# Kernel tuning notes

Hardware: AMD Instinct MI355X
Metric: run time of the kernel (lower is better)

## Reference

```python
import jax, jax.numpy as jnp
import numpy as np
import math


def _conv1x1(x, w, b):
    # x: [B,C,H,W], w: [O,C], b: [O] -> [B,O,H,W]
    return jnp.einsum('oc,bchw->bohw', w, x) + b[None, :, None, None]


def _attn_branch(x, f_w, f_b, g_w, g_b, h_w, h_b, gamma):
    B, C, H, W = x.shape
    N = H * W
    k_dim = C // 8
    f = _conv1x1(x, f_w, f_b).reshape(B, k_dim, N)  # [B,k,N]
    g = _conv1x1(x, g_w, g_b).reshape(B, k_dim, N)  # [B,k,N]
    # attention[b, n, m] = sum_k f[b,k,n] * g[b,k,m] / sqrt(k_dim)
    scores = jnp.einsum('bkn,bkm->bnm', f, g) / math.sqrt(k_dim)
    attn = jax.nn.softmax(scores, axis=2)  # softmax over last dim (dim=2)
    h = _conv1x1(x, h_w, h_b).reshape(B, C, N)  # [B,C,N]
    sa_map = jnp.einsum('bcn,bnm->bcm', h, attn).reshape(B, C, H, W)
    return gamma[0] * sa_map + x


def setup_inputs() -> dict:
    key = jax.random.key(0)
    ks = jax.random.split(key, 8)
    B, C, H, W = 4, 256, 64, 64
    kd = C // 8
    scale_in = 1.0 / math.sqrt(C)
    return {
        'x1': jax.random.normal(ks[0], (B, C, H, W), jnp.float32),
        'x2': jax.random.normal(ks[1], (B, C, H, W), jnp.float32),
        'f_w': jax.random.normal(ks[2], (kd, C), jnp.float32) * scale_in,
        'f_b': jnp.zeros((kd,), jnp.float32),
        'g_w': jax.random.normal(ks[3], (kd, C), jnp.float32) * scale_in,
        'g_b': jnp.zeros((kd,), jnp.float32),
        'h1_w': jax.random.normal(ks[4], (C, C), jnp.float32) * scale_in,
        'h1_b': jnp.zeros((C,), jnp.float32),
        'h2_w': jax.random.normal(ks[5], (C, C), jnp.float32) * scale_in,
        'h2_b': jnp.zeros((C,), jnp.float32),
        'gamma1': jax.random.normal(ks[6], (1,), jnp.float32),
        'gamma2': jax.random.normal(ks[7], (1,), jnp.float32),
    }


def reference(x1, x2, f_w, f_b, g_w, g_b, h1_w, h1_b, h2_w, h2_b, gamma1, gamma2):
    y1 = _attn_branch(x1, f_w, f_b, g_w, g_b, h1_w, h1_b, gamma1)
    y2 = _attn_branch(x2, f_w, f_b, g_w, g_b, h2_w, h2_b, gamma2)
    return (y1, y2)
```

## Files before the change

kernel.cpp:

```cpp
#include <hip/hip_runtime.h>
#include <math.h>

#define NDIM 4096
#define CDIM 256
#define KD   32
#define SCALE 0.17677669529663687f
#define SHIFT 8.0f

typedef __attribute__((ext_vector_type(8))) short short8;
typedef __attribute__((ext_vector_type(4))) float f32x4;
typedef unsigned short u16;
typedef unsigned int u32;

__device__ __forceinline__ u32 f2bf(float x) {
  union { float f; u32 u; } v; v.f = x;
  return (v.u + 0x7FFFu + ((v.u >> 16) & 1u)) >> 16;
}

#define MFMA16(a, b, c) __builtin_amdgcn_mfma_f32_16x16x32_bf16((a), (b), (c), 0, 0, 0)

__global__ void cast_all_kernel(const float* __restrict__ h1w,
                                const float* __restrict__ h2w,
                                const float* __restrict__ fw,
                                const float* __restrict__ gw,
                                u16* __restrict__ dst) {
  int i = blockIdx.x * 256 + threadIdx.x;
  float v;
  if (i < 65536) v = h1w[i];
  else if (i < 131072) v = h2w[i - 65536];
  else if (i < 139264) v = fw[i - 131072];
  else v = gw[i - 139264];
  dst[i] = (u16)f2bf(v);
}

__global__ __launch_bounds__(256) void transpose_cast_kernel(
    const float* __restrict__ x1, const float* __restrict__ x2,
    u16* __restrict__ xt) {
  __shared__ float ts[64][68];
  const int t = threadIdx.x;
  const int ntile = blockIdx.x * 64, Ctile = blockIdx.y * 64, z = blockIdx.z;
  const float* xb = ((z >> 2) ? x2 : x1) + (size_t)(z & 3) * CDIM * NDIM;
  u16* xtb = xt + (size_t)z * NDIM * CDIM;
  const int r = t >> 4, c4 = (t & 15) * 4;
#pragma unroll
  for (int i = 0; i < 4; i++) {
    float4 v = *(const float4*)&xb[(size_t)(Ctile + r + i * 16) * NDIM + ntile + c4];
    *(float4*)&ts[r + i * 16][c4] = v;
  }
  __syncthreads();
  const int n = t >> 2, Cg = (t & 3) * 16;
  u32 pk[8];
#pragma unroll
  for (int j = 0; j < 8; j++) {
    u32 lo = f2bf(ts[Cg + 2 * j][n]);
    u32 hi = f2bf(ts[Cg + 2 * j + 1][n]);
    pk[j] = lo | (hi << 16);
  }
  uint4* dst = (uint4*)&xtb[(size_t)(ntile + n) * CDIM + Ctile + Cg];
  dst[0] = make_uint4(pk[0], pk[1], pk[2], pk[3]);
  dst[1] = make_uint4(pk[4], pk[5], pk[6], pk[7]);
}

__global__ __launch_bounds__(256) void conv_fg_kernel(
    const u16* __restrict__ Wf, const float* __restrict__ fbias,
    const u16* __restrict__ Wg, const float* __restrict__ gbias,
    const u16* __restrict__ xt, u16* __restrict__ ftT, u16* __restrict__ gtT) {
  const int t = threadIdx.x, w = t >> 6, l = t & 63, li = l & 15, q = l >> 4;
  const int ntile = blockIdx.x * 64, bb = blockIdx.y;
  const u16* xtb = xt + (size_t)bb * NDIM * CDIM;
  f32x4 zero4 = {0.f, 0.f, 0.f, 0.f};
  f32x4 acc[2][2];
  for (int i = 0; i < 2; i++) for (int j = 0; j < 2; j++) acc[i][j] = zero4;
  const int nrow = ntile + w * 16 + li;

  for (int k0 = 0; k0 < CDIM; k0 += 32) {
    short8 bx = *(const short8*)&xtb[(size_t)nrow * CDIM + k0 + q * 8];
    short8 af0 = *(const short8*)&Wf[(size_t)(li) * CDIM + k0 + q * 8];
    short8 af1 = *(const short8*)&Wf[(size_t)(16 + li) * CDIM + k0 + q * 8];
    short8 ag0 = *(const short8*)&Wg[(size_t)(li) * CDIM + k0 + q * 8];
    short8 ag1 = *(const short8*)&Wg[(size_t)(16 + li) * CDIM + k0 + q * 8];
    acc[0][0] = MFMA16(af0, bx, acc[0][0]);
    acc[0][1] = MFMA16(af1, bx, acc[0][1]);
    acc[1][0] = MFMA16(ag0, bx, acc[1][0]);
    acc[1][1] = MFMA16(ag1, bx, acc[1][1]);
  }
  u16* outs[2] = {ftT + (size_t)bb * NDIM * KD, gtT + (size_t)bb * NDIM * KD};
  const float* biases[2] = {fbias, gbias};
#pragma unroll
  for (int fg = 0; fg < 2; fg++) {
#pragma unroll
    for (int os = 0; os < 2; os++) {
      float b0 = biases[fg][os * 16 + q * 4 + 0];
      float b1 = biases[fg][os * 16 + q * 4 + 1];
      float b2 = biases[fg][os * 16 + q * 4 + 2];
      float b3 = biases[fg][os * 16 + q * 4 + 3];
      u32 p0 = f2bf(acc[fg][os][0] + b0) | (f2bf(acc[fg][os][1] + b1) << 16);
      u32 p1 = f2bf(acc[fg][os][2] + b2) | (f2bf(acc[fg][os][3] + b3) << 16);
      *(uint2*)&outs[fg][(size_t)nrow * KD + os * 16 + q * 4] = make_uint2(p0, p1);
    }
  }
}

__global__ __launch_bounds__(256) void conv_h_kernel(
    const u16* __restrict__ Wall, const float* __restrict__ b1,
    const float* __restrict__ b2, const u16* __restrict__ xt,
    u16* __restrict__ outH) {
  const int t = threadIdx.x, w = t >> 6, l = t & 63, li = l & 15, q = l >> 4;
  const int ntile = blockIdx.x * 64;
  const int o0 = blockIdx.y * 64 + w * 16;
  const int bb = blockIdx.z, branch = bb >> 2;
  const u16* W = Wall + (size_t)branch * CDIM * CDIM;
  const float* bias = branch ? b2 : b1;
  const u16* xtb = xt + (size_t)bb * NDIM * CDIM;
  u16* ob = outH + (size_t)bb * CDIM * NDIM;
  f32x4 zero4 = {0.f, 0.f, 0.f, 0.f};
  f32x4 acc[4];
  for (int i = 0; i < 4; i++) acc[i] = zero4;

  for (int k0 = 0; k0 < CDIM; k0 += 32) {
    short8 a = *(const short8*)&W[(size_t)(o0 + li) * CDIM + k0 + q * 8];
#pragma unroll
    for (int ns = 0; ns < 4; ns++) {
      short8 bf = *(const short8*)&xtb[(size_t)(ntile + ns * 16 + li) * CDIM + k0 + q * 8];
      acc[ns] = MFMA16(a, bf, acc[ns]);
    }
  }
  float bv[4];
#pragma unroll
  for (int reg = 0; reg < 4; reg++) bv[reg] = bias[o0 + q * 4 + reg];
#pragma unroll
  for (int ns = 0; ns < 4; ns++) {
    int n = ntile + ns * 16 + li;
#pragma unroll
    for (int reg = 0; reg < 4; reg++) {
      int c = o0 + q * 4 + reg;
      ob[(size_t)c * NDIM + n] = (u16)f2bf(acc[ns][reg] + bv[reg]);
    }
  }
}

__global__ __launch_bounds__(256) void stats_kernel(
    const u16* __restrict__ ft, const u16* __restrict__ gt,
    float* __restrict__ L) {
  __shared__ float zred[32][64];
  const int t = threadIdx.x, w = t >> 6, l = t & 63, li = l & 15, q = l >> 4;
  const int n0 = blockIdx.x * 32;
  const int bb = blockIdx.z * 4 + blockIdx.y;
  const u16* ftb = ft + (size_t)bb * NDIM * KD;
  const u16* gtb = gt + (size_t)bb * NDIM * KD;
  f32x4 zero4 = {0.f, 0.f, 0.f, 0.f};

  short8 a0 = *(const short8*)&ftb[(size_t)(n0 + li) * KD + q * 8];
  short8 a1 = *(const short8*)&ftb[(size_t)(n0 + 16 + li) * KD + q * 8];
  f32x4 z0 = zero4, z1 = zero4;

#pragma unroll 2
  for (int it = 0; it < 64; it++) {
    int m = (it * 4 + w) * 16;
    short8 bf = *(const short8*)&gtb[(size_t)(m + li) * KD + q * 8];
    f32x4 S0 = MFMA16(a0, bf, zero4);
    f32x4 S1 = MFMA16(a1, bf, zero4);
#pragma unroll
    for (int reg = 0; reg < 4; reg++) {
      z0[reg] += __expf(S0[reg] * SCALE - SHIFT);
      z1[reg] += __expf(S1[reg] * SCALE - SHIFT);
    }
  }
#pragma unroll
  for (int reg = 0; reg < 4; reg++) {
    zred[q * 4 + reg][w * 16 + li] = z0[reg];
    zred[16 + q * 4 + reg][w * 16 + li] = z1[reg];
  }
  __syncthreads();
  const int r = t >> 3, i8 = t & 7;
  float4 s1 = *(const float4*)&zred[r][i8 * 8];
  float4 s2 = *(const float4*)&zred[r][i8 * 8 + 4];
  float sum = s1.x + s1.y + s1.z + s1.w + s2.x + s2.y + s2.z + s2.w;
  sum += __shfl_xor(sum, 1, 8);
  sum += __shfl_xor(sum, 2, 8);
  sum += __shfl_xor(sum, 4, 8);
  if (i8 == 0) L[(size_t)bb * NDIM + n0 + r] = SHIFT + __logf(sum);
}

__global__ __launch_bounds__(512, 4) void apply_kernel(
    const u16* __restrict__ ft, const u16* __restrict__ gt,
    const u16* __restrict__ h, const float* __restrict__ L,
    const float* __restrict__ x1, const float* __restrict__ x2,
    const float* __restrict__ gamma1, const float* __restrict__ gamma2,
    float* __restrict__ out) {
  __shared__ u16 Pt[2][64][72];
  const int t = threadIdx.x, w = t >> 6, l = t & 63, li = l & 15, q = l >> 4;
  const int mtile = blockIdx.x * 64;
  const int b = blockIdx.y, br = blockIdx.z, bb = br * 4 + b;
  const u16* ftb = ft + (size_t)bb * NDIM * KD;
  const u16* gtb = gt + (size_t)bb * NDIM * KD;
  const u16* hb = h + (size_t)bb * CDIM * NDIM;
  const float* Lb = L + (size_t)bb * NDIM;
  const float* xb = (br ? x2 : x1) + (size_t)b * CDIM * NDIM;
  const float gmv = br ? gamma2[0] : gamma1[0];
  float* ob = out + (size_t)bb * CDIM * NDIM;

  const int msub_s = w >> 1, npair = w & 1;
  const int c0 = w * 32;
  f32x4 zero4 = {0.f, 0.f, 0.f, 0.f};
  short8 gfrag = *(const short8*)&gtb[(size_t)(mtile + msub_s * 16 + li) * KD + q * 8];

  f32x4 acc[2][4];
  for (int i = 0; i < 2; i++) for (int j = 0; j < 4; j++) acc[i][j] = zero4;

  u32 Ppk[2][2];
  short8 afA[2];
  f32x4 LA[2];
  {
#pragma unroll
    for (int j = 0; j < 2; j++) {
      int n = (npair * 2 + j) * 16;
      short8 a = *(const short8*)&ftb[(size_t)(n + li) * KD + q * 8];
      f32x4 l4 = *(const f32x4*)&Lb[n + q * 4];
      f32x4 S = MFMA16(a, gfrag, zero4);
      Ppk[j][0] = f2bf(__expf(S[0] * SCALE - l4[0])) |
                  (f2bf(__expf(S[1] * SCALE - l4[1])) << 16);
      Ppk[j][1] = f2bf(__expf(S[2] * SCALE - l4[2])) |
                  (f2bf(__expf(S[3] * SCALE - l4[3])) << 16);
    }
#pragma unroll
    for (int j = 0; j < 2; j++) {
      int n = 64 + (npair * 2 + j) * 16;
      afA[j] = *(const short8*)&ftb[(size_t)(n + li) * KD + q * 8];
      LA[j] = *(const f32x4*)&Lb[n + q * 4];
    }
  }

  for (int i = 0; i < 64; i++) {
    const int n0 = i * 64;
    const int buf = i & 1;
    short8 ah[2][2];
#pragma unroll
    for (int cs = 0; cs < 2; cs++)
#pragma unroll
      for (int kh = 0; kh < 2; kh++)
        ah[cs][kh] = *(const short8*)
            &hb[(size_t)(c0 + cs * 16 + li) * NDIM + n0 + kh * 32 + q * 8];

#pragma unroll
    for (int j = 0; j < 2; j++)
      *(uint2*)&Pt[buf][msub_s * 16 + li][(npair * 2 + j) * 16 + q * 4] =
          make_uint2(Ppk[j][0], Ppk[j][1]);

#pragma unroll
    for (int j = 0; j < 2; j++) {
      f32x4 S = MFMA16(afA[j], gfrag, zero4);
      Ppk[j][0] = f2bf(__expf(S[0] * SCALE - LA[j][0])) |
                  (f2bf(__expf(S[1] * SCALE - LA[j][1])) << 16);
      Ppk[j][1] = f2bf(__expf(S[2] * SCALE - LA[j][2])) |
                  (f2bf(__expf(S[3] * SCALE - LA[j][3])) << 16);
    }

    __syncthreads();

    {
      int ch2 = (i + 2 < 64) ? i + 2 : 63;
#pragma unroll
      for (int j = 0; j < 2; j++) {
        int n = ch2 * 64 + (npair * 2 + j) * 16;
        afA[j] = *(const short8*)&ftb[(size_t)(n + li) * KD + q * 8];
        LA[j] = *(const f32x4*)&Lb[n + q * 4];
      }
    }

#pragma unroll
    for (int kh = 0; kh < 2; kh++) {
#pragma unroll
      for (int ms = 0; ms < 4; ms++) {
        short8 bm = *(const short8*)&Pt[buf][ms * 16 + li][kh * 32 + q * 8];
        acc[0][ms] = MFMA16(ah[0][kh], bm, acc[0][ms]);
        acc[1][ms] = MFMA16(ah[1][kh], bm, acc[1][ms]);
      }
    }
  }

#pragma unroll
  for (int cs = 0; cs < 2; cs++) {
#pragma unroll
    for (int ms = 0; ms < 4; ms++) {
#pragma unroll
      for (int reg = 0; reg < 4; reg++) {
        int c = c0 + cs * 16 + q * 4 + reg;
        int m = mtile + ms * 16 + li;
        size_t idx = (size_t)c * NDIM + m;
        ob[idx] = gmv * acc[cs][ms][reg] + xb[idx];
      }
    }
  }
}

extern "C" void kernel_launch(void* const* d_in, const int* in_sizes, int n_in,
                              void* d_out, int out_size, void* d_ws, size_t ws_size,
                              hipStream_t stream) {
  const float* x1 = (const float*)d_in[0];
  const float* x2 = (const float*)d_in[1];
  const float* f_w = (const float*)d_in[2];
  const float* f_b = (const float*)d_in[3];
  const float* g_w = (const float*)d_in[4];
  const float* g_b = (const float*)d_in[5];
  const float* h1_w = (const float*)d_in[6];
  const float* h1_b = (const float*)d_in[7];
  const float* h2_w = (const float*)d_in[8];
  const float* h2_b = (const float*)d_in[9];
  const float* gamma1 = (const float*)d_in[10];
  const float* gamma2 = (const float*)d_in[11];
  float* out = (float*)d_out;

  char* ws = (char*)d_ws;
  u16* xt  = (u16*)(ws);
  u16* wh  = (u16*)(ws + 16777216);
  u16* ftw = (u16*)(ws + 33554432);
  u16* gtw = (u16*)(ws + 35651584);
  u16* wWh = (u16*)(ws + 37748736);
  u16* wWf = (u16*)(ws + 38010880);
  u16* wWg = (u16*)(ws + 38027264);
  float* Lw = (float*)(ws + 38043648);

  cast_all_kernel<<<576, 256, 0, stream>>>(h1_w, h2_w, f_w, g_w, wWh);

  transpose_cast_kernel<<<dim3(64, 4, 8), 256, 0, stream>>>(x1, x2, xt);

  conv_fg_kernel<<<dim3(64, 8), 256, 0, stream>>>(wWf, f_b, wWg, g_b, xt, ftw, gtw);
  conv_h_kernel<<<dim3(64, 4, 8), 256, 0, stream>>>(wWh, h1_b, h2_b, xt, wh);

  stats_kernel<<<dim3(128, 4, 2), 256, 0, stream>>>(ftw, gtw, Lw);

  apply_kernel<<<dim3(64, 4, 2), 512, 0, stream>>>(ftw, gtw, wh, Lw, x1, x2,
                                                   gamma1, gamma2, out);
}
```

Before: 344.3 us.

## Split apply over N halves with atomic accumulation and fold softmax normalizer into h

The attention apply kernel now splits the reduction over n into two halves, doubling the grid (512 blocks) and accumulating into the output with atomicAdd, after a new kernel pre-initializes the output with the residual x. The per-row log-sum normalizer is folded into the h projection by scaling h by exp(-L) in conv_h, which now runs after stats. This removes the L loads and subtraction from the inner exp loop. The cost is an extra full-output copy pass, float atomics on 8M outputs, nondeterministic summation order, and a risk of exp(S*scale) overflow precision in bf16 without the shift.

```diff
diff --git a/kernel.cpp b/kernel.cpp
--- a/kernel.cpp
+++ b/kernel.cpp
@@ -33,6 +33,15 @@
   dst[i] = (u16)f2bf(v);
 }
 
+__global__ void init_out_kernel(const float* __restrict__ x1,
+                                const float* __restrict__ x2,
+                                float4* __restrict__ out) {
+  int i = blockIdx.x * 256 + threadIdx.x;
+  const int half = 1 << 20;
+  float4 v = (i < half) ? ((const float4*)x1)[i] : ((const float4*)x2)[i - half];
+  out[i] = v;
+}
+
 __global__ __launch_bounds__(256) void transpose_cast_kernel(
     const float* __restrict__ x1, const float* __restrict__ x2,
     u16* __restrict__ xt) {
@@ -101,44 +110,6 @@
   }
 }
 
-__global__ __launch_bounds__(256) void conv_h_kernel(
-    const u16* __restrict__ Wall, const float* __restrict__ b1,
-    const float* __restrict__ b2, const u16* __restrict__ xt,
-    u16* __restrict__ outH) {
-  const int t = threadIdx.x, w = t >> 6, l = t & 63, li = l & 15, q = l >> 4;
-  const int ntile = blockIdx.x * 64;
-  const int o0 = blockIdx.y * 64 + w * 16;
-  const int bb = blockIdx.z, branch = bb >> 2;
-  const u16* W = Wall + (size_t)branch * CDIM * CDIM;
-  const float* bias = branch ? b2 : b1;
-  const u16* xtb = xt + (size_t)bb * NDIM * CDIM;
-  u16* ob = outH + (size_t)bb * CDIM * NDIM;
-  f32x4 zero4 = {0.f, 0.f, 0.f, 0.f};
-  f32x4 acc[4];
-  for (int i = 0; i < 4; i++) acc[i] = zero4;
-
-  for (int k0 = 0; k0 < CDIM; k0 += 32) {
-    short8 a = *(const short8*)&W[(size_t)(o0 + li) * CDIM + k0 + q * 8];
-#pragma unroll
-    for (int ns = 0; ns < 4; ns++) {
-      short8 bf = *(const short8*)&xtb[(size_t)(ntile + ns * 16 + li) * CDIM + k0 + q * 8];
-      acc[ns] = MFMA16(a, bf, acc[ns]);
-    }
-  }
-  float bv[4];
-#pragma unroll
-  for (int reg = 0; reg < 4; reg++) bv[reg] = bias[o0 + q * 4 + reg];
-#pragma unroll
-  for (int ns = 0; ns < 4; ns++) {
-    int n = ntile + ns * 16 + li;
-#pragma unroll
-    for (int reg = 0; reg < 4; reg++) {
-      int c = o0 + q * 4 + reg;
-      ob[(size_t)c * NDIM + n] = (u16)f2bf(acc[ns][reg] + bv[reg]);
-    }
-  }
-}
-
 __global__ __launch_bounds__(256) void stats_kernel(
     const u16* __restrict__ ft, const u16* __restrict__ gt,
     float* __restrict__ L) {
@@ -182,21 +153,60 @@
   if (i8 == 0) L[(size_t)bb * NDIM + n0 + r] = SHIFT + __logf(sum);
 }
 
-__global__ __launch_bounds__(512, 4) void apply_kernel(
+__global__ __launch_bounds__(256) void conv_h_kernel(
+    const u16* __restrict__ Wall, const float* __restrict__ b1,
+    const float* __restrict__ b2, const u16* __restrict__ xt,
+    const float* __restrict__ L, u16* __restrict__ outH) {
+  const int t = threadIdx.x, w = t >> 6, l = t & 63, li = l & 15, q = l >> 4;
+  const int ntile = blockIdx.x * 64;
+  const int o0 = blockIdx.y * 64 + w * 16;
+  const int bb = blockIdx.z, branch = bb >> 2;
+  const u16* W = Wall + (size_t)branch * CDIM * CDIM;
+  const float* bias = branch ? b2 : b1;
+  const u16* xtb = xt + (size_t)bb * NDIM * CDIM;
+  const float* Lb = L + (size_t)bb * NDIM;
+  u16* ob = outH + (size_t)bb * CDIM * NDIM;
+  f32x4 zero4 = {0.f, 0.f, 0.f, 0.f};
+  f32x4 acc[4];
+  for (int i = 0; i < 4; i++) acc[i] = zero4;
+
+  for (int k0 = 0; k0 < CDIM; k0 += 32) {
+    short8 a = *(const short8*)&W[(size_t)(o0 + li) * CDIM + k0 + q * 8];
+#pragma unroll
+    for (int ns = 0; ns < 4; ns++) {
+      short8 bf = *(const short8*)&xtb[(size_t)(ntile + ns * 16 + li) * CDIM + k0 + q * 8];
+      acc[ns] = MFMA16(a, bf, acc[ns]);
+    }
+  }
+  float bv[4];
+#pragma unroll
+  for (int reg = 0; reg < 4; reg++) bv[reg] = bias[o0 + q * 4 + reg];
+#pragma unroll
+  for (int ns = 0; ns < 4; ns++) {
+    int n = ntile + ns * 16 + li;
+    float ex = __expf(-Lb[n]);
+#pragma unroll
+    for (int reg = 0; reg < 4; reg++) {
+      int c = o0 + q * 4 + reg;
+      ob[(size_t)c * NDIM + n] = (u16)f2bf((acc[ns][reg] + bv[reg]) * ex);
+    }
+  }
+}
+
+__global__ __launch_bounds__(512, 6) void apply_kernel(
     const u16* __restrict__ ft, const u16* __restrict__ gt,
-    const u16* __restrict__ h, const float* __restrict__ L,
-    const float* __restrict__ x1, const float* __restrict__ x2,
+    const u16* __restrict__ h,
     const float* __restrict__ gamma1, const float* __restrict__ gamma2,
     float* __restrict__ out) {
   __shared__ u16 Pt[2][64][72];
   const int t = threadIdx.x, w = t >> 6, l = t & 63, li = l & 15, q = l >> 4;
   const int mtile = blockIdx.x * 64;
-  const int b = blockIdx.y, br = blockIdx.z, bb = br * 4 + b;
+  const int b = blockIdx.y >> 1, nh = blockIdx.y & 1;
+  const int br = blockIdx.z, bb = br * 4 + b;
+  const int nbase = nh * 2048;
   const u16* ftb = ft + (size_t)bb * NDIM * KD;
   const u16* gtb = gt + (size_t)bb * NDIM * KD;
   const u16* hb = h + (size_t)bb * CDIM * NDIM;
-  const float* Lb = L + (size_t)bb * NDIM;
-  const float* xb = (br ? x2 : x1) + (size_t)b * CDIM * NDIM;
   const float gmv = br ? gamma2[0] : gamma1[0];
   float* ob = out + (size_t)bb * CDIM * NDIM;
 
@@ -210,29 +220,24 @@
 
   u32 Ppk[2][2];
   short8 afA[2];
-  f32x4 LA[2];
   {
 #pragma unroll
     for (int j = 0; j < 2; j++) {
-      int n = (npair * 2 + j) * 16;
+      int n = nbase + (npair * 2 + j) * 16;
       short8 a = *(const short8*)&ftb[(size_t)(n + li) * KD + q * 8];
-      f32x4 l4 = *(const f32x4*)&Lb[n + q * 4];
       f32x4 S = MFMA16(a, gfrag, zero4);
-      Ppk[j][0] = f2bf(__expf(S[0] * SCALE - l4[0])) |
-                  (f2bf(__expf(S[1] * SCALE - l4[1])) << 16);
-      Ppk[j][1] = f2bf(__expf(S[2] * SCALE - l4[2])) |
-                  (f2bf(__expf(S[3] * SCALE - l4[3])) << 16);
+      Ppk[j][0] = f2bf(__expf(S[0] * SCALE)) | (f2bf(__expf(S[1] * SCALE)) << 16);
+      Ppk[j][1] = f2bf(__expf(S[2] * SCALE)) | (f2bf(__expf(S[3] * SCALE)) << 16);
     }
 #pragma unroll
     for (int j = 0; j < 2; j++) {
-      int n = 64 + (npair * 2 + j) * 16;
+      int n = nbase + 64 + (npair * 2 + j) * 16;
       afA[j] = *(const short8*)&ftb[(size_t)(n + li) * KD + q * 8];
-      LA[j] = *(const f32x4*)&Lb[n + q * 4];
-    }
-  }
-
-  for (int i = 0; i < 64; i++) {
-    const int n0 = i * 64;
+    }
+  }
+
+  for (int i = 0; i < 32; i++) {
+    const int n0 = nbase + i * 64;
     const int buf = i & 1;
     short8 ah[2][2];
 #pragma unroll
@@ -250,21 +255,18 @@
 #pragma unroll
     for (int j = 0; j < 2; j++) {
       f32x4 S = MFMA16(afA[j], gfrag, zero4);
-      Ppk[j][0] = f2bf(__expf(S[0] * SCALE - LA[j][0])) |
-                  (f2bf(__expf(S[1] * SCALE - LA[j][1])) << 16);
-      Ppk[j][1] = f2bf(__expf(S[2] * SCALE - LA[j][2])) |
-                  (f2bf(__expf(S[3] * SCALE - LA[j][3])) << 16);
+      Ppk[j][0] = f2bf(__expf(S[0] * SCALE)) | (f2bf(__expf(S[1] * SCALE)) << 16);
+      Ppk[j][1] = f2bf(__expf(S[2] * SCALE)) | (f2bf(__expf(S[3] * SCALE)) << 16);
     }
 
     __syncthreads();
 
     {
-      int ch2 = (i + 2 < 64) ? i + 2 : 63;
+      int ch2 = (i + 2 < 32) ? i + 2 : 31;
 #pragma unroll
       for (int j = 0; j < 2; j++) {
-        int n = ch2 * 64 + (npair * 2 + j) * 16;
+        int n = nbase + ch2 * 64 + (npair * 2 + j) * 16;
         afA[j] = *(const short8*)&ftb[(size_t)(n + li) * KD + q * 8];
-        LA[j] = *(const f32x4*)&Lb[n + q * 4];
       }
     }
 
@@ -287,8 +289,7 @@
       for (int reg = 0; reg < 4; reg++) {
         int c = c0 + cs * 16 + q * 4 + reg;
         int m = mtile + ms * 16 + li;
-        size_t idx = (size_t)c * NDIM + m;
-        ob[idx] = gmv * acc[cs][ms][reg] + xb[idx];
+        atomicAdd(&ob[(size_t)c * NDIM + m], gmv * acc[cs][ms][reg]);
       }
     }
   }
@@ -323,13 +324,16 @@
 
   cast_all_kernel<<<576, 256, 0, stream>>>(h1_w, h2_w, f_w, g_w, wWh);
 
+  init_out_kernel<<<8192, 256, 0, stream>>>(x1, x2, (float4*)out);
+
   transpose_cast_kernel<<<dim3(64, 4, 8), 256, 0, stream>>>(x1, x2, xt);
 
   conv_fg_kernel<<<dim3(64, 8), 256, 0, stream>>>(wWf, f_b, wWg, g_b, xt, ftw, gtw);
-  conv_h_kernel<<<dim3(64, 4, 8), 256, 0, stream>>>(wWh, h1_b, h2_b, xt, wh);
 
   stats_kernel<<<dim3(128, 4, 2), 256, 0, stream>>>(ftw, gtw, Lw);
 
-  apply_kernel<<<dim3(64, 4, 2), 512, 0, stream>>>(ftw, gtw, wh, Lw, x1, x2,
+  conv_h_kernel<<<dim3(64, 4, 8), 256, 0, stream>>>(wWh, h1_b, h2_b, xt, Lw, wh);
+
+  apply_kernel<<<dim3(64, 8, 2), 512, 0, stream>>>(ftw, gtw, wh,
                                                    gamma1, gamma2, out);
 }
```

Result: slower. 363.3 us (+5.5%).

## Fold softmax normalizer into h projection and double-buffer h loads in apply

Applied to the files above, without the earlier changes.

The per-row normalizer exp(-L[n]) now scales h inside conv_h, which runs after the stats kernel, so apply no longer loads L or subtracts it before each exp. The apply loop is unrolled by two so the h fragments for the next tile are prefetched into alternating register sets, and __syncthreads is replaced by an inline-asm waitcnt plus s_barrier. The aim is to cut per-element ALU work and hide global-load latency in the hot loop. The cost is extra registers and a bf16 rounding of the pre-scaled h values, which may shift numerics slightly.

```diff
diff --git a/kernel.cpp b/kernel.cpp
--- a/kernel.cpp
+++ b/kernel.cpp
@@ -101,44 +101,6 @@
   }
 }
 
-__global__ __launch_bounds__(256) void conv_h_kernel(
-    const u16* __restrict__ Wall, const float* __restrict__ b1,
-    const float* __restrict__ b2, const u16* __restrict__ xt,
-    u16* __restrict__ outH) {
-  const int t = threadIdx.x, w = t >> 6, l = t & 63, li = l & 15, q = l >> 4;
-  const int ntile = blockIdx.x * 64;
-  const int o0 = blockIdx.y * 64 + w * 16;
-  const int bb = blockIdx.z, branch = bb >> 2;
-  const u16* W = Wall + (size_t)branch * CDIM * CDIM;
-  const float* bias = branch ? b2 : b1;
-  const u16* xtb = xt + (size_t)bb * NDIM * CDIM;
-  u16* ob = outH + (size_t)bb * CDIM * NDIM;
-  f32x4 zero4 = {0.f, 0.f, 0.f, 0.f};
-  f32x4 acc[4];
-  for (int i = 0; i < 4; i++) acc[i] = zero4;
-
-  for (int k0 = 0; k0 < CDIM; k0 += 32) {
-    short8 a = *(const short8*)&W[(size_t)(o0 + li) * CDIM + k0 + q * 8];
-#pragma unroll
-    for (int ns = 0; ns < 4; ns++) {
-      short8 bf = *(const short8*)&xtb[(size_t)(ntile + ns * 16 + li) * CDIM + k0 + q * 8];
-      acc[ns] = MFMA16(a, bf, acc[ns]);
-    }
-  }
-  float bv[4];
-#pragma unroll
-  for (int reg = 0; reg < 4; reg++) bv[reg] = bias[o0 + q * 4 + reg];
-#pragma unroll
-  for (int ns = 0; ns < 4; ns++) {
-    int n = ntile + ns * 16 + li;
-#pragma unroll
-    for (int reg = 0; reg < 4; reg++) {
-      int c = o0 + q * 4 + reg;
-      ob[(size_t)c * NDIM + n] = (u16)f2bf(acc[ns][reg] + bv[reg]);
-    }
-  }
-}
-
 __global__ __launch_bounds__(256) void stats_kernel(
     const u16* __restrict__ ft, const u16* __restrict__ gt,
     float* __restrict__ L) {
@@ -182,9 +144,49 @@
   if (i8 == 0) L[(size_t)bb * NDIM + n0 + r] = SHIFT + __logf(sum);
 }
 
+__global__ __launch_bounds__(256) void conv_h_kernel(
+    const u16* __restrict__ Wall, const float* __restrict__ b1,
+    const float* __restrict__ b2, const u16* __restrict__ xt,
+    const float* __restrict__ L, u16* __restrict__ outH) {
+  const int t = threadIdx.x, w = t >> 6, l = t & 63, li = l & 15, q = l >> 4;
+  const int ntile = blockIdx.x * 64;
+  const int o0 = blockIdx.y * 64 + w * 16;
+  const int bb = blockIdx.z, branch = bb >> 2;
+  const u16* W = Wall + (size_t)branch * CDIM * CDIM;
+  const float* bias = branch ? b2 : b1;
+  const u16* xtb = xt + (size_t)bb * NDIM * CDIM;
+  const float* Lb = L + (size_t)bb * NDIM;
+  u16* ob = outH + (size_t)bb * CDIM * NDIM;
+  f32x4 zero4 = {0.f, 0.f, 0.f, 0.f};
+  f32x4 acc[4];
+  for (int i = 0; i < 4; i++) acc[i] = zero4;
+
+  for (int k0 = 0; k0 < CDIM; k0 += 32) {
+    short8 a = *(const short8*)&W[(size_t)(o0 + li) * CDIM + k0 + q * 8];
+#pragma unroll
+    for (int ns = 0; ns < 4; ns++) {
+      short8 bf = *(const short8*)&xtb[(size_t)(ntile + ns * 16 + li) * CDIM + k0 + q * 8];
+      acc[ns] = MFMA16(a, bf, acc[ns]);
+    }
+  }
+  float bv[4];
+#pragma unroll
+  for (int reg = 0; reg < 4; reg++) bv[reg] = bias[o0 + q * 4 + reg];
+#pragma unroll
+  for (int ns = 0; ns < 4; ns++) {
+    int n = ntile + ns * 16 + li;
+    float ex = __expf(-Lb[n]);
+#pragma unroll
+    for (int reg = 0; reg < 4; reg++) {
+      int c = o0 + q * 4 + reg;
+      ob[(size_t)c * NDIM + n] = (u16)f2bf((acc[ns][reg] + bv[reg]) * ex);
+    }
+  }
+}
+
 __global__ __launch_bounds__(512, 4) void apply_kernel(
     const u16* __restrict__ ft, const u16* __restrict__ gt,
-    const u16* __restrict__ h, const float* __restrict__ L,
+    const u16* __restrict__ h,
     const float* __restrict__ x1, const float* __restrict__ x2,
     const float* __restrict__ gamma1, const float* __restrict__ gamma2,
     float* __restrict__ out) {
@@ -195,7 +197,6 @@
   const u16* ftb = ft + (size_t)bb * NDIM * KD;
   const u16* gtb = gt + (size_t)bb * NDIM * KD;
   const u16* hb = h + (size_t)bb * CDIM * NDIM;
-  const float* Lb = L + (size_t)bb * NDIM;
   const float* xb = (br ? x2 : x1) + (size_t)b * CDIM * NDIM;
   const float gmv = br ? gamma2[0] : gamma1[0];
   float* ob = out + (size_t)bb * CDIM * NDIM;
@@ -210,74 +211,69 @@
 
   u32 Ppk[2][2];
   short8 afA[2];
-  f32x4 LA[2];
-  {
-#pragma unroll
-    for (int j = 0; j < 2; j++) {
-      int n = (npair * 2 + j) * 16;
-      short8 a = *(const short8*)&ftb[(size_t)(n + li) * KD + q * 8];
-      f32x4 l4 = *(const f32x4*)&Lb[n + q * 4];
-      f32x4 S = MFMA16(a, gfrag, zero4);
-      Ppk[j][0] = f2bf(__expf(S[0] * SCALE - l4[0])) |
-                  (f2bf(__expf(S[1] * SCALE - l4[1])) << 16);
-      Ppk[j][1] = f2bf(__expf(S[2] * SCALE - l4[2])) |
-                  (f2bf(__expf(S[3] * SCALE - l4[3])) << 16);
-    }
-#pragma unroll
-    for (int j = 0; j < 2; j++) {
-      int n = 64 + (npair * 2 + j) * 16;
-      afA[j] = *(const short8*)&ftb[(size_t)(n + li) * KD + q * 8];
-      LA[j] = *(const f32x4*)&Lb[n + q * 4];
-    }
-  }
-
-  for (int i = 0; i < 64; i++) {
-    const int n0 = i * 64;
-    const int buf = i & 1;
-    short8 ah[2][2];
-#pragma unroll
-    for (int cs = 0; cs < 2; cs++)
-#pragma unroll
-      for (int kh = 0; kh < 2; kh++)
-        ah[cs][kh] = *(const short8*)
-            &hb[(size_t)(c0 + cs * 16 + li) * NDIM + n0 + kh * 32 + q * 8];
-
-#pragma unroll
-    for (int j = 0; j < 2; j++)
-      *(uint2*)&Pt[buf][msub_s * 16 + li][(npair * 2 + j) * 16 + q * 4] =
-          make_uint2(Ppk[j][0], Ppk[j][1]);
-
-#pragma unroll
-    for (int j = 0; j < 2; j++) {
-      f32x4 S = MFMA16(afA[j], gfrag, zero4);
-      Ppk[j][0] = f2bf(__expf(S[0] * SCALE - LA[j][0])) |
-                  (f2bf(__expf(S[1] * SCALE - LA[j][1])) << 16);
-      Ppk[j][1] = f2bf(__expf(S[2] * SCALE - LA[j][2])) |
-                  (f2bf(__expf(S[3] * SCALE - LA[j][3])) << 16);
-    }
-
-    __syncthreads();
-
-    {
-      int ch2 = (i + 2 < 64) ? i + 2 : 63;
-#pragma unroll
-      for (int j = 0; j < 2; j++) {
-        int n = ch2 * 64 + (npair * 2 + j) * 16;
-        afA[j] = *(const short8*)&ftb[(size_t)(n + li) * KD + q * 8];
-        LA[j] = *(const f32x4*)&Lb[n + q * 4];
-      }
-    }
-
-#pragma unroll
-    for (int kh = 0; kh < 2; kh++) {
-#pragma unroll
-      for (int ms = 0; ms < 4; ms++) {
-        short8 bm = *(const short8*)&Pt[buf][ms * 16 + li][kh * 32 + q * 8];
-        acc[0][ms] = MFMA16(ah[0][kh], bm, acc[0][ms]);
-        acc[1][ms] = MFMA16(ah[1][kh], bm, acc[1][ms]);
-      }
-    }
-  }
+  short8 ahA[2][2], ahB[2][2];
+
+#pragma unroll
+  for (int j = 0; j < 2; j++) {
+    int n = (npair * 2 + j) * 16;
+    short8 a = *(const short8*)&ftb[(size_t)(n + li) * KD + q * 8];
+    f32x4 S = MFMA16(a, gfrag, zero4);
+    Ppk[j][0] = f2bf(__expf(S[0] * SCALE)) | (f2bf(__expf(S[1] * SCALE)) << 16);
+    Ppk[j][1] = f2bf(__expf(S[2] * SCALE)) | (f2bf(__expf(S[3] * SCALE)) << 16);
+  }
+#pragma unroll
+  for (int j = 0; j < 2; j++)
+    afA[j] = *(const short8*)&ftb[(size_t)(64 + (npair * 2 + j) * 16 + li) * KD + q * 8];
+#pragma unroll
+  for (int cs = 0; cs < 2; cs++)
+#pragma unroll
+    for (int kh = 0; kh < 2; kh++)
+      ahA[cs][kh] = *(const short8*)
+          &hb[(size_t)(c0 + cs * 16 + li) * NDIM + kh * 32 + q * 8];
+
+#define APPLY_BODY(I, AH_USE, AH_LOAD)                                         \
+  {                                                                            \
+    const int buf = (I) & 1;                                                   \
+    _Pragma("unroll")                                                          \
+    for (int j = 0; j < 2; j++)                                                \
+      *(uint2*)&Pt[buf][msub_s * 16 + li][(npair * 2 + j) * 16 + q * 4] =      \
+          make_uint2(Ppk[j][0], Ppk[j][1]);                                    \
+    _Pragma("unroll")                                                          \
+    for (int j = 0; j < 2; j++) {                                              \
+      f32x4 S = MFMA16(afA[j], gfrag, zero4);                                  \
+      Ppk[j][0] = f2bf(__expf(S[0] * SCALE)) | (f2bf(__expf(S[1] * SCALE)) << 16); \
+      Ppk[j][1] = f2bf(__expf(S[2] * SCALE)) | (f2bf(__expf(S[3] * SCALE)) << 16); \
+    }                                                                          \
+    asm volatile("s_waitcnt lgkmcnt(0)\n\ts_barrier" ::: "memory");            \
+    {                                                                          \
+      const int ch2 = ((I) + 2 < 64) ? (I) + 2 : 63;                           \
+      _Pragma("unroll")                                                        \
+      for (int j = 0; j < 2; j++)                                              \
+        afA[j] = *(const short8*)                                              \
+            &ftb[(size_t)(ch2 * 64 + (npair * 2 + j) * 16 + li) * KD + q * 8]; \
+      const int n1 = (((I) + 1 < 64) ? (I) + 1 : 63) * 64;                     \
+      _Pragma("unroll")                                                        \
+      for (int cs = 0; cs < 2; cs++)                                           \
+        _Pragma("unroll")                                                      \
+        for (int kh = 0; kh < 2; kh++)                                         \
+          AH_LOAD[cs][kh] = *(const short8*)                                   \
+              &hb[(size_t)(c0 + cs * 16 + li) * NDIM + n1 + kh * 32 + q * 8];  \
+    }                                                                          \
+    _Pragma("unroll")                                                          \
+    for (int kh = 0; kh < 2; kh++)                                             \
+      _Pragma("unroll")                                                        \
+      for (int ms = 0; ms < 4; ms++) {                                         \
+        short8 bm = *(const short8*)&Pt[buf][ms * 16 + li][kh * 32 + q * 8];   \
+        acc[0][ms] = MFMA16(AH_USE[0][kh], bm, acc[0][ms]);                    \
+        acc[1][ms] = MFMA16(AH_USE[1][kh], bm, acc[1][ms]);                    \
+      }                                                                        \
+  }
+
+  for (int i = 0; i < 64; i += 2) {
+    APPLY_BODY(i, ahA, ahB)
+    APPLY_BODY(i + 1, ahB, ahA)
+  }
+#undef APPLY_BODY
 
 #pragma unroll
   for (int cs = 0; cs < 2; cs++) {
@@ -326,10 +322,11 @@
   transpose_cast_kernel<<<dim3(64, 4, 8), 256, 0, stream>>>(x1, x2, xt);
 
   conv_fg_kernel<<<dim3(64, 8), 256, 0, stream>>>(wWf, f_b, wWg, g_b, xt, ftw, gtw);
-  conv_h_kernel<<<dim3(64, 4, 8), 256, 0, stream>>>(wWh, h1_b, h2_b, xt, wh);
 
   stats_kernel<<<dim3(128, 4, 2), 256, 0, stream>>>(ftw, gtw, Lw);
 
-  apply_kernel<<<dim3(64, 4, 2), 512, 0, stream>>>(ftw, gtw, wh, Lw, x1, x2,
+  conv_h_kernel<<<dim3(64, 4, 8), 256, 0, stream>>>(wWh, h1_b, h2_b, xt, Lw, wh);
+
+  apply_kernel<<<dim3(64, 4, 2), 512, 0, stream>>>(ftw, gtw, wh, x1, x2,
                                                    gamma1, gamma2, out);
 }
```

Result: no change. 344.8 us (+0.1%).

## Fold softmax normalizer into h conv and widen apply tile to 128 columns

Applied to the files above, without the earlier changes.

The per-row softmax normalizer exp(-L[n]) now scales the h projection inside the conv_h epilogue, and conv_h runs after the stats kernel. The apply kernel therefore computes unnormalized exp(S*scale) and no longer loads or subtracts L. The apply block grows to 1024 threads covering 128 output columns, which halves the number of times each h tile is re-read from memory. The change also packs bf16 pairs with the HIP intrinsic. In exchange it drops the max-style shift from the exponent, which risks overflow for large scores, and the larger block may raise register pressure.

```diff
diff --git a/kernel.cpp b/kernel.cpp
--- a/kernel.cpp
+++ b/kernel.cpp
@@ -1,4 +1,5 @@
 #include <hip/hip_runtime.h>
+#include <hip/hip_bf16.h>
 #include <math.h>
 
 #define NDIM 4096
@@ -15,6 +16,13 @@
 __device__ __forceinline__ u32 f2bf(float x) {
   union { float f; u32 u; } v; v.f = x;
   return (v.u + 0x7FFFu + ((v.u >> 16) & 1u)) >> 16;
+}
+
+__device__ __forceinline__ u32 pack_bf16x2(float a, float b) {
+  __hip_bfloat162 h2 = __float22bfloat162_rn(make_float2(a, b));
+  u32 r;
+  __builtin_memcpy(&r, &h2, 4);
+  return r;
 }
 
 #define MFMA16(a, b, c) __builtin_amdgcn_mfma_f32_16x16x32_bf16((a), (b), (c), 0, 0, 0)
@@ -101,44 +109,6 @@
   }
 }
 
-__global__ __launch_bounds__(256) void conv_h_kernel(
-    const u16* __restrict__ Wall, const float* __restrict__ b1,
-    const float* __restrict__ b2, const u16* __restrict__ xt,
-    u16* __restrict__ outH) {
-  const int t = threadIdx.x, w = t >> 6, l = t & 63, li = l & 15, q = l >> 4;
-  const int ntile = blockIdx.x * 64;
-  const int o0 = blockIdx.y * 64 + w * 16;
-  const int bb = blockIdx.z, branch = bb >> 2;
-  const u16* W = Wall + (size_t)branch * CDIM * CDIM;
-  const float* bias = branch ? b2 : b1;
-  const u16* xtb = xt + (size_t)bb * NDIM * CDIM;
-  u16* ob = outH + (size_t)bb * CDIM * NDIM;
-  f32x4 zero4 = {0.f, 0.f, 0.f, 0.f};
-  f32x4 acc[4];
-  for (int i = 0; i < 4; i++) acc[i] = zero4;
-
-  for (int k0 = 0; k0 < CDIM; k0 += 32) {
-    short8 a = *(const short8*)&W[(size_t)(o0 + li) * CDIM + k0 + q * 8];
-#pragma unroll
-    for (int ns = 0; ns < 4; ns++) {
-      short8 bf = *(const short8*)&xtb[(size_t)(ntile + ns * 16 + li) * CDIM + k0 + q * 8];
-      acc[ns] = MFMA16(a, bf, acc[ns]);
-    }
-  }
-  float bv[4];
-#pragma unroll
-  for (int reg = 0; reg < 4; reg++) bv[reg] = bias[o0 + q * 4 + reg];
-#pragma unroll
-  for (int ns = 0; ns < 4; ns++) {
-    int n = ntile + ns * 16 + li;
-#pragma unroll
-    for (int reg = 0; reg < 4; reg++) {
-      int c = o0 + q * 4 + reg;
-      ob[(size_t)c * NDIM + n] = (u16)f2bf(acc[ns][reg] + bv[reg]);
-    }
-  }
-}
-
 __global__ __launch_bounds__(256) void stats_kernel(
     const u16* __restrict__ ft, const u16* __restrict__ gt,
     float* __restrict__ L) {
@@ -182,26 +152,66 @@
   if (i8 == 0) L[(size_t)bb * NDIM + n0 + r] = SHIFT + __logf(sum);
 }
 
-__global__ __launch_bounds__(512, 4) void apply_kernel(
+__global__ __launch_bounds__(256) void conv_h_kernel(
+    const u16* __restrict__ Wall, const float* __restrict__ b1,
+    const float* __restrict__ b2, const u16* __restrict__ xt,
+    const float* __restrict__ L, u16* __restrict__ outH) {
+  const int t = threadIdx.x, w = t >> 6, l = t & 63, li = l & 15, q = l >> 4;
+  const int ntile = blockIdx.x * 64;
+  const int o0 = blockIdx.y * 64 + w * 16;
+  const int bb = blockIdx.z, branch = bb >> 2;
+  const u16* W = Wall + (size_t)branch * CDIM * CDIM;
+  const float* bias = branch ? b2 : b1;
+  const u16* xtb = xt + (size_t)bb * NDIM * CDIM;
+  const float* Lb = L + (size_t)bb * NDIM;
+  u16* ob = outH + (size_t)bb * CDIM * NDIM;
+  f32x4 zero4 = {0.f, 0.f, 0.f, 0.f};
+  f32x4 acc[4];
+  for (int i = 0; i < 4; i++) acc[i] = zero4;
+
+  for (int k0 = 0; k0 < CDIM; k0 += 32) {
+    short8 a = *(const short8*)&W[(size_t)(o0 + li) * CDIM + k0 + q * 8];
+#pragma unroll
+    for (int ns = 0; ns < 4; ns++) {
+      short8 bf = *(const short8*)&xtb[(size_t)(ntile + ns * 16 + li) * CDIM + k0 + q * 8];
+      acc[ns] = MFMA16(a, bf, acc[ns]);
+    }
+  }
+  float bv[4];
+#pragma unroll
+  for (int reg = 0; reg < 4; reg++) bv[reg] = bias[o0 + q * 4 + reg];
+#pragma unroll
+  for (int ns = 0; ns < 4; ns++) {
+    int n = ntile + ns * 16 + li;
+    float ex = __expf(-Lb[n]);
+#pragma unroll
+    for (int reg = 0; reg < 4; reg++) {
+      int c = o0 + q * 4 + reg;
+      ob[(size_t)c * NDIM + n] = (u16)f2bf((acc[ns][reg] + bv[reg]) * ex);
+    }
+  }
+}
+
+__global__ __launch_bounds__(1024, 4) void apply_kernel(
     const u16* __restrict__ ft, const u16* __restrict__ gt,
-    const u16* __restrict__ h, const float* __restrict__ L,
+    const u16* __restrict__ h,
     const float* __restrict__ x1, const float* __restrict__ x2,
     const float* __restrict__ gamma1, const float* __restrict__ gamma2,
     float* __restrict__ out) {
-  __shared__ u16 Pt[2][64][72];
+  __shared__ u16 Pt[2][128][72];
   const int t = threadIdx.x, w = t >> 6, l = t & 63, li = l & 15, q = l >> 4;
-  const int mtile = blockIdx.x * 64;
+  const int mtile = blockIdx.x * 128;
   const int b = blockIdx.y, br = blockIdx.z, bb = br * 4 + b;
   const u16* ftb = ft + (size_t)bb * NDIM * KD;
   const u16* gtb = gt + (size_t)bb * NDIM * KD;
   const u16* hb = h + (size_t)bb * CDIM * NDIM;
-  const float* Lb = L + (size_t)bb * NDIM;
   const float* xb = (br ? x2 : x1) + (size_t)b * CDIM * NDIM;
   const float gmv = br ? gamma2[0] : gamma1[0];
   float* ob = out + (size_t)bb * CDIM * NDIM;
 
   const int msub_s = w >> 1, npair = w & 1;
-  const int c0 = w * 32;
+  const int c0 = (w & 7) * 32;
+  const int mg = (w >> 3) * 64;
   f32x4 zero4 = {0.f, 0.f, 0.f, 0.f};
   short8 gfrag = *(const short8*)&gtb[(size_t)(mtile + msub_s * 16 + li) * KD + q * 8];
 
@@ -210,26 +220,17 @@
 
   u32 Ppk[2][2];
   short8 afA[2];
-  f32x4 LA[2];
-  {
-#pragma unroll
-    for (int j = 0; j < 2; j++) {
-      int n = (npair * 2 + j) * 16;
-      short8 a = *(const short8*)&ftb[(size_t)(n + li) * KD + q * 8];
-      f32x4 l4 = *(const f32x4*)&Lb[n + q * 4];
-      f32x4 S = MFMA16(a, gfrag, zero4);
-      Ppk[j][0] = f2bf(__expf(S[0] * SCALE - l4[0])) |
-                  (f2bf(__expf(S[1] * SCALE - l4[1])) << 16);
-      Ppk[j][1] = f2bf(__expf(S[2] * SCALE - l4[2])) |
-                  (f2bf(__expf(S[3] * SCALE - l4[3])) << 16);
-    }
-#pragma unroll
-    for (int j = 0; j < 2; j++) {
-      int n = 64 + (npair * 2 + j) * 16;
-      afA[j] = *(const short8*)&ftb[(size_t)(n + li) * KD + q * 8];
-      LA[j] = *(const f32x4*)&Lb[n + q * 4];
-    }
-  }
+#pragma unroll
+  for (int j = 0; j < 2; j++) {
+    int n = (npair * 2 + j) * 16;
+    short8 a = *(const short8*)&ftb[(size_t)(n + li) * KD + q * 8];
+    f32x4 S = MFMA16(a, gfrag, zero4);
+    Ppk[j][0] = pack_bf16x2(__expf(S[0] * SCALE), __expf(S[1] * SCALE));
+    Ppk[j][1] = pack_bf16x2(__expf(S[2] * SCALE), __expf(S[3] * SCALE));
+  }
+#pragma unroll
+  for (int j = 0; j < 2; j++)
+    afA[j] = *(const short8*)&ftb[(size_t)(64 + (npair * 2 + j) * 16 + li) * KD + q * 8];
 
   for (int i = 0; i < 64; i++) {
     const int n0 = i * 64;
@@ -250,10 +251,8 @@
 #pragma unroll
     for (int j = 0; j < 2; j++) {
       f32x4 S = MFMA16(afA[j], gfrag, zero4);
-      Ppk[j][0] = f2bf(__expf(S[0] * SCALE - LA[j][0])) |
-                  (f2bf(__expf(S[1] * SCALE - LA[j][1])) << 16);
-      Ppk[j][1] = f2bf(__expf(S[2] * SCALE - LA[j][2])) |
-                  (f2bf(__expf(S[3] * SCALE - LA[j][3])) << 16);
+      Ppk[j][0] = pack_bf16x2(__expf(S[0] * SCALE), __expf(S[1] * SCALE));
+      Ppk[j][1] = pack_bf16x2(__expf(S[2] * SCALE), __expf(S[3] * SCALE));
     }
 
     __syncthreads();
@@ -264,7 +263,6 @@
       for (int j = 0; j < 2; j++) {
         int n = ch2 * 64 + (npair * 2 + j) * 16;
         afA[j] = *(const short8*)&ftb[(size_t)(n + li) * KD + q * 8];
-        LA[j] = *(const f32x4*)&Lb[n + q * 4];
       }
     }
 
@@ -272,7 +270,7 @@
     for (int kh = 0; kh < 2; kh++) {
 #pragma unroll
       for (int ms = 0; ms < 4; ms++) {
-        short8 bm = *(const short8*)&Pt[buf][ms * 16 + li][kh * 32 + q * 8];
+        short8 bm = *(const short8*)&Pt[buf][mg + ms * 16 + li][kh * 32 + q * 8];
         acc[0][ms] = MFMA16(ah[0][kh], bm, acc[0][ms]);
         acc[1][ms] = MFMA16(ah[1][kh], bm, acc[1][ms]);
       }
@@ -286,7 +284,7 @@
 #pragma unroll
       for (int reg = 0; reg < 4; reg++) {
         int c = c0 + cs * 16 + q * 4 + reg;
-        int m = mtile + ms * 16 + li;
+        int m = mtile + mg + ms * 16 + li;
         size_t idx = (size_t)c * NDIM + m;
         ob[idx] = gmv * acc[cs][ms][reg] + xb[idx];
       }
@@ -326,10 +324,11 @@
   transpose_cast_kernel<<<dim3(64, 4, 8), 256, 0, stream>>>(x1, x2, xt);
 
   conv_fg_kernel<<<dim3(64, 8), 256, 0, stream>>>(wWf, f_b, wWg, g_b, xt, ftw, gtw);
-  conv_h_kernel<<<dim3(64, 4, 8), 256, 0, stream>>>(wWh, h1_b, h2_b, xt, wh);
 
   stats_kernel<<<dim3(128, 4, 2), 256, 0, stream>>>(ftw, gtw, Lw);
 
-  apply_kernel<<<dim3(64, 4, 2), 512, 0, stream>>>(ftw, gtw, wh, Lw, x1, x2,
-                                                   gamma1, gamma2, out);
-}
+  conv_h_kernel<<<dim3(64, 4, 8), 256, 0, stream>>>(wWh, h1_b, h2_b, xt, Lw, wh);
+
+  apply_kernel<<<dim3(32, 4, 2), 1024, 0, stream>>>(ftw, gtw, wh, x1, x2,
+                                                    gamma1, gamma2, out);
+}
```

After: 332.3 us. 1.04x faster.
